# Kernel tuning notes

Measured on AMD Instinct MI355X. Metric: run time of the kernel, lower is better.

## Reference

```python
import jax, jax.numpy as jnp
import numpy as np

WS = 8          # window size
SS = 4          # shift size
NH = 4          # num heads
DIM = 128
RPE_HID = 512
MLP_HID = 512   # 4 * DIM
EPS = 1e-5


def _rel_coords_table(ws):
    h = np.arange(-(ws - 1), ws, dtype=np.float32)
    tbl = np.stack(np.meshgrid(h, h, indexing='ij'), axis=-1)  # [2ws-1, 2ws-1, 2]
    tbl = tbl / (ws - 1) * 8.0
    tbl = np.sign(tbl) * np.log2(np.abs(tbl) + 1.0) / np.log2(8.0)
    return jnp.asarray(tbl, dtype=jnp.float32)


def _rel_pos_index(ws):
    coords = np.stack(np.meshgrid(np.arange(ws), np.arange(ws), indexing='ij'))  # [2, ws, ws]
    cf = coords.reshape(2, -1)
    rel = (cf[:, :, None] - cf[:, None, :]).transpose(1, 2, 0).astype(np.int64)  # [N, N, 2]
    rel[..., 0] += ws - 1
    rel[..., 1] += ws - 1
    rel[..., 0] *= 2 * ws - 1
    return jnp.asarray(rel.sum(-1))  # [N, N]


def _attn_mask(H, W, ws, ss):
    img = np.zeros((H, W), np.float32)
    cnt = 0
    for hsl in (slice(0, -ws), slice(-ws, -ss), slice(-ss, None)):
        for wsl in (slice(0, -ws), slice(-ws, -ss), slice(-ss, None)):
            img[hsl, wsl] = cnt
            cnt += 1
    mw = img.reshape(H // ws, ws, W // ws, ws).transpose(0, 2, 1, 3).reshape(-1, ws * ws)
    diff = mw[:, None, :] - mw[:, :, None]
    return jnp.asarray(np.where(diff != 0, -100.0, 0.0).astype(np.float32))  # [nW, N, N]


def _layernorm(x, w, b):
    mu = x.mean(-1, keepdims=True)
    var = ((x - mu) ** 2).mean(-1, keepdims=True)
    return (x - mu) * jax.lax.rsqrt(var + EPS) * w + b


def setup_inputs() -> dict:
    key = jax.random.key(0)
    ks = jax.random.split(key, 16)
    s = 0.02
    return {
        'x': jax.random.normal(ks[0], (32, 4096, DIM), jnp.float32),
        'qkv_w': jax.random.normal(ks[1], (3 * DIM, DIM), jnp.float32) * s,
        'qkv_b': jnp.zeros((3 * DIM,), jnp.float32),
        'proj_w': jax.random.normal(ks[2], (DIM, DIM), jnp.float32) * s,
        'proj_b': jnp.zeros((DIM,), jnp.float32),
        'rpe_w1': jax.random.normal(ks[3], (RPE_HID, 2), jnp.float32) * s,
        'rpe_b1': jnp.zeros((RPE_HID,), jnp.float32),
        'rpe_w2': jax.random.normal(ks[4], (NH, RPE_HID), jnp.float32) * s,
        'norm1_w': jnp.ones((DIM,), jnp.float32),
        'norm1_b': jnp.zeros((DIM,), jnp.float32),
        'fc1_w': jax.random.normal(ks[5], (MLP_HID, DIM), jnp.float32) * s,
        'fc1_b': jnp.zeros((MLP_HID,), jnp.float32),
        'fc2_w': jax.random.normal(ks[6], (DIM, MLP_HID), jnp.float32) * s,
        'fc2_b': jnp.zeros((DIM,), jnp.float32),
        'norm2_w': jnp.ones((DIM,), jnp.float32),
        'norm2_b': jnp.zeros((DIM,), jnp.float32),
        'H': 64,
        'W': 64,
    }


def reference(x, qkv_w, qkv_b, proj_w, proj_b, rpe_w1, rpe_b1, rpe_w2,
              norm1_w, norm1_b, fc1_w, fc1_b, fc2_w, fc2_b, norm2_w, norm2_b, H, W):
    B, L, C = x.shape
    N = WS * WS
    hd = C // NH
    scale = hd ** -0.5
    nWh, nWw = H // WS, W // WS
    nW = nWh * nWw

    # ---- shifted window partition ----
    xs = x.reshape(B, H, W, C)
    xs = jnp.roll(xs, shift=(-SS, -SS), axis=(1, 2))
    xw = xs.reshape(B, nWh, WS, nWw, WS, C).transpose(0, 1, 3, 2, 4, 5).reshape(-1, N, C)

    # ---- window attention ----
    qkv = xw @ qkv_w.T + qkv_b                              # [B*nW, N, 3C]
    qkv = qkv.reshape(-1, N, 3, NH, hd).transpose(2, 0, 3, 1, 4)
    q, k, v = qkv[0], qkv[1], qkv[2]                        # [B*nW, NH, N, hd]
    attn = jnp.einsum('whnd,whmd->whnm', q * scale, k)      # [B*nW, NH, N, N]

    # continuous relative position bias via MLP on log-spaced coords
    tbl = _rel_coords_table(WS)                             # [2ws-1, 2ws-1, 2]
    t = jax.nn.relu(tbl @ rpe_w1.T + rpe_b1) @ rpe_w2.T     # [2ws-1, 2ws-1, NH]
    t = t.reshape(-1, NH)
    rel_idx = _rel_pos_index(WS)                            # [N, N]
    bias = t[rel_idx].transpose(2, 0, 1)                    # [NH, N, N]
    attn = attn + bias[None]

    # shift mask
    mask = _attn_mask(H, W, WS, SS)                         # [nW, N, N]
    attn = attn.reshape(B, nW, NH, N, N) + mask[None, :, None]
    attn = jax.nn.softmax(attn, axis=-1).reshape(-1, NH, N, N)

    out = jnp.einsum('whnm,whmd->whnd', attn, v)            # [B*nW, NH, N, hd]
    out = out.transpose(0, 2, 1, 3).reshape(-1, N, C)
    out = out @ proj_w.T + proj_b

    # ---- window reverse + unshift ----
    out = out.reshape(B, nWh, nWw, WS, WS, C).transpose(0, 1, 3, 2, 4, 5).reshape(B, H, W, C)
    out = jnp.roll(out, shift=(SS, SS), axis=(1, 2)).reshape(B, L, C)

    # ---- post-norm residual ----
    x = x + _layernorm(out, norm1_w, norm1_b)

    # ---- MLP (GELU exact) + post-norm residual ----
    h = jax.nn.gelu(x @ fc1_w.T + fc1_b, approximate=False)
    h = h @ fc2_w.T + fc2_b
    x = x + _layernorm(h, norm2_w, norm2_b)
    return x
```

## Files before the change

kernel.cpp:

```cpp
#include <hip/hip_runtime.h>
#include <hip/hip_bf16.h>

typedef __attribute__((ext_vector_type(8))) short short8_t;
typedef __attribute__((ext_vector_type(4))) float f32x4_t;
typedef __attribute__((ext_vector_type(2))) float f32x2_t;

#define NHEAD 4
#define SCALE 0.17677669529663687f

#define OFF_W    0L
#define OFF_TBL  393216L
#define OFF_QKV  458752L
#define OFF_X1   458752L
#define OFF_H    67567616L
#define OFF_ATTN 101122048L
#define OFF_PROJ 134676480L

__device__ __forceinline__ unsigned short f2bf(float f){
  unsigned int u = __float_as_uint(f);
  u += 0x7FFFu + ((u >> 16) & 1u);
  return (unsigned short)(u >> 16);
}
__device__ __forceinline__ float bf2f(unsigned short s){
  return __uint_as_float(((unsigned int)s) << 16);
}

__device__ __forceinline__ int win_row_to_orig(int r){
  int win = r >> 6, n = r & 63;
  int b = win >> 6, wh = (win >> 3) & 7, ww = win & 7;
  int hs = wh*8 + (n >> 3), wsv = ww*8 + (n & 7);
  return (b << 12) + (((hs + 4) & 63) << 6) + ((wsv + 4) & 63);
}

__global__ __launch_bounds__(256) void prep_kernel(
    const float* __restrict__ qkv_w, const float* __restrict__ proj_w,
    const float* __restrict__ fc1_w, const float* __restrict__ fc2_w,
    const float* __restrict__ rpe_w1, const float* __restrict__ rpe_b1,
    const float* __restrict__ rpe_w2,
    unsigned short* __restrict__ wbf, float* __restrict__ tbl)
{
  if (blockIdx.x == 0) {
    int t = threadIdx.x;
    if (t < 225) {
      int a = t / 15, b = t % 15;
      float v0 = (float)(a - 7) * (8.0f / 7.0f);
      float v1 = (float)(b - 7) * (8.0f / 7.0f);
      float c0 = (v0 > 0.f ? 1.f : (v0 < 0.f ? -1.f : 0.f)) * log2f(fabsf(v0) + 1.f) * (1.0f/3.0f);
      float c1 = (v1 > 0.f ? 1.f : (v1 < 0.f ? -1.f : 0.f)) * log2f(fabsf(v1) + 1.f) * (1.0f/3.0f);
      float a0 = 0.f, a1 = 0.f, a2 = 0.f, a3 = 0.f;
      for (int k = 0; k < 512; k++){
        float h = c0 * rpe_w1[2*k] + c1 * rpe_w1[2*k+1] + rpe_b1[k];
        h = fmaxf(h, 0.f);
        a0 += h * rpe_w2[k];
        a1 += h * rpe_w2[512 + k];
        a2 += h * rpe_w2[1024 + k];
        a3 += h * rpe_w2[1536 + k];
      }
      tbl[t] = a0; tbl[225 + t] = a1; tbl[450 + t] = a2; tbl[675 + t] = a3;
    }
  } else {
    int e = (blockIdx.x - 1) * 256 + threadIdx.x;
    float v;
    if (e < 49152)       v = qkv_w[e];
    else if (e < 65536)  v = proj_w[e - 49152];
    else if (e < 131072) v = fc1_w[e - 65536];
    else                 v = fc2_w[e - 131072];
    wbf[e] = f2bf(v);
  }
}

template<int N, int K, int AMODE, int EPI>
__global__ __launch_bounds__(256) void gemm_kernel(
    const void* __restrict__ Ap, const unsigned short* __restrict__ Bw,
    const float* __restrict__ bias, void* __restrict__ Out)
{
  constexpr int NT = N / 16;
  constexpr int KC = K / 32;
  __shared__ __align__(16) unsigned short bs[N * 40];
  int lane = threadIdx.x & 63;
  int wave = threadIdx.x >> 6;
  int m0 = blockIdx.x * 64 + wave * 16;
  int l15 = lane & 15;
  int kg  = lane >> 4;
  int arow = m0 + l15;
  int ag = (AMODE == 1) ? win_row_to_orig(arow) : arow;

  f32x4_t acc[NT];
#pragma unroll
  for (int t = 0; t < NT; t++) acc[t] = (f32x4_t){0.f, 0.f, 0.f, 0.f};

  for (int kc = 0; kc < KC; ++kc){
    if (kc) __syncthreads();
    for (int e = threadIdx.x; e < N * 4; e += 256){
      int n = e >> 2, k8 = e & 3;
      short8_t v = *(const short8_t*)(Bw + n * K + kc * 32 + k8 * 8);
      *(short8_t*)(&bs[n * 40 + k8 * 8]) = v;
    }
    __syncthreads();

    short8_t af;
    if (AMODE == 2) {
      af = *(const short8_t*)((const unsigned short*)Ap + (long)ag * K + kc * 32 + kg * 8);
    } else {
      const float* ap = (const float*)Ap + (long)ag * K + kc * 32 + kg * 8;
      f32x4_t a0 = *(const f32x4_t*)ap;
      f32x4_t a1 = *(const f32x4_t*)(ap + 4);
      union { short8_t v; unsigned short u[8]; } pk;
      pk.u[0] = f2bf(a0[0]); pk.u[1] = f2bf(a0[1]); pk.u[2] = f2bf(a0[2]); pk.u[3] = f2bf(a0[3]);
      pk.u[4] = f2bf(a1[0]); pk.u[5] = f2bf(a1[1]); pk.u[6] = f2bf(a1[2]); pk.u[7] = f2bf(a1[3]);
      af = pk.v;
    }
#pragma unroll
    for (int t = 0; t < NT; t++){
      short8_t bf = *(const short8_t*)(&bs[(t * 16 + l15) * 40 + kg * 8]);
      acc[t] = __builtin_amdgcn_mfma_f32_16x16x32_bf16(af, bf, acc[t], 0, 0, 0);
    }
  }

  int orow[4];
#pragma unroll
  for (int i = 0; i < 4; i++){
    int r = m0 + kg * 4 + i;
    orow[i] = (EPI == 1) ? win_row_to_orig(r) : r;
  }
#pragma unroll
  for (int t = 0; t < NT; t++){
    int col = t * 16 + l15;
    float bv = bias[col];
#pragma unroll
    for (int i = 0; i < 4; i++){
      float v = acc[t][i] + bv;
      if (EPI == 0) {
        ((unsigned short*)Out)[(long)orow[i] * N + col] = f2bf(v);
      } else if (EPI == 1) {
        ((float*)Out)[(long)orow[i] * N + col] = v;
      } else if (EPI == 2) {
        float g = 0.5f * v * (1.f + erff(v * 0.70710678118f));
        ((unsigned short*)Out)[(long)orow[i] * N + col] = f2bf(g);
      } else {
        ((float*)Out)[(long)orow[i] * N + col] = v;
      }
    }
  }
}

__global__ __launch_bounds__(256) void attn_kernel(
    const unsigned short* __restrict__ qkv, const float* __restrict__ tbl,
    unsigned short* __restrict__ outp)
{
  __shared__ __align__(16) unsigned short vt[NHEAD][32][72];
  __shared__ __align__(16) unsigned short pl[NHEAD][16][72];
  __shared__ float tl[900];
  int win  = blockIdx.x;
  int head = threadIdx.x >> 6;
  int lane = threadIdx.x & 63;
  int l15 = lane & 15, kg = lane >> 4;

  for (int e = threadIdx.x; e < 900; e += 256) tl[e] = tbl[e];

  const unsigned short* qbase = qkv + (long)win * 64 * 384;

  {
    const unsigned short* vp = qbase + lane * 384 + 256 + head * 32;
#pragma unroll
    for (int d0 = 0; d0 < 4; d0++){
      union { short8_t v; unsigned short u[8]; } pk;
      pk.v = *(const short8_t*)(vp + d0 * 8);
#pragma unroll
      for (int j = 0; j < 8; j++)
        vt[head][d0 * 8 + j][lane] = pk.u[j];
    }
  }

  short8_t kf[4];
#pragma unroll
  for (int nt = 0; nt < 4; nt++)
    kf[nt] = *(const short8_t*)(qbase + (nt * 16 + l15) * 384 + 128 + head * 32 + kg * 8);

  __syncthreads();

  short8_t bvf[2][2];
#pragma unroll
  for (int dt = 0; dt < 2; dt++)
#pragma unroll
    for (int ks = 0; ks < 2; ks++)
      bvf[dt][ks] = *(const short8_t*)(&vt[head][dt * 16 + l15][ks * 32 + kg * 8]);

  const float* tlh = tl + head * 225;
  bool wh7 = ((win >> 3) & 7) == 7;
  bool ww7 = (win & 7) == 7;
  bool crq_lt = (kg & 1) == 0;
  bool crm_lt = (l15 & 7) < 4;
  int  t3m_lo = l15 >> 3;
  int  dj0 = (kg & 1) * 4 - (l15 & 7) + 7;

#pragma unroll
  for (int mt = 0; mt < 4; mt++){
    short8_t qf = *(const short8_t*)(qbase + (mt * 16 + l15) * 384 + head * 32 + kg * 8);
    f32x4_t sacc[4];
#pragma unroll
    for (int nt = 0; nt < 4; nt++)
      sacc[nt] = __builtin_amdgcn_mfma_f32_16x16x32_bf16(qf, kf[nt], (f32x4_t){0.f,0.f,0.f,0.f}, 0, 0, 0);

    int t3q = mt * 2 + (kg >> 1);
    bool rrq_lt = t3q < 4;
    float p[4][4];
#pragma unroll
    for (int nt = 0; nt < 4; nt++){
      int t3m = nt * 2 + t3m_lo;
      const float* bp = tlh + (t3q - t3m + 7) * 15 + dj0;
      bool masked = (wh7 && (rrq_lt != (t3m < 4))) || (ww7 && (crq_lt != crm_lt));
      float mterm = masked ? -100.f : 0.f;
#pragma unroll
      for (int ii = 0; ii < 4; ii++){
        float s = sacc[nt][ii] * SCALE + bp[ii] + mterm;
        p[nt][ii] = __expf(s);
      }
    }
    float inv[4];
#pragma unroll
    for (int ii = 0; ii < 4; ii++){
      float sm = (p[0][ii] + p[1][ii]) + (p[2][ii] + p[3][ii]);
      sm += __shfl_xor(sm, 1); sm += __shfl_xor(sm, 2);
      sm += __shfl_xor(sm, 4); sm += __shfl_xor(sm, 8);
      inv[ii] = 1.f / sm;
    }
#pragma unroll
    for (int nt = 0; nt < 4; nt++)
#pragma unroll
      for (int ii = 0; ii < 4; ii++)
        pl[head][kg * 4 + ii][nt * 16 + l15] = f2bf(p[nt][ii]);

    asm volatile("s_waitcnt lgkmcnt(0)" ::: "memory");

    f32x4_t oacc[2] = {{0.f,0.f,0.f,0.f},{0.f,0.f,0.f,0.f}};
#pragma unroll
    for (int ks = 0; ks < 2; ks++){
      short8_t pa = *(const short8_t*)(&pl[head][l15][ks * 32 + kg * 8]);
#pragma unroll
      for (int dt = 0; dt < 2; dt++)
        oacc[dt] = __builtin_amdgcn_mfma_f32_16x16x32_bf16(pa, bvf[dt][ks], oacc[dt], 0, 0, 0);
    }

    unsigned short* op = outp + ((long)(win * 64 + mt * 16 + kg * 4)) * 128 + head * 32;
#pragma unroll
    for (int ii = 0; ii < 4; ii++)
#pragma unroll
      for (int dt = 0; dt < 2; dt++)
        op[ii * 128 + dt * 16 + l15] = f2bf(oacc[dt][ii] * inv[ii]);
  }
}

__global__ __launch_bounds__(256) void ln_residual_kernel(
    const float* in, const float* __restrict__ res,
    const float* __restrict__ w, const float* __restrict__ b, float* out)
{
  int row = blockIdx.x * 4 + (threadIdx.x >> 6);
  int lane = threadIdx.x & 63;
  long base = (long)row * 128 + lane * 2;
  f32x2_t v = *(const f32x2_t*)(in + base);
  float sm = v[0] + v[1];
#pragma unroll
  for (int off = 1; off < 64; off <<= 1) sm += __shfl_xor(sm, off);
  float mu = sm * 0.0078125f;
  float d0 = v[0] - mu, d1 = v[1] - mu;
  float qv = d0 * d0 + d1 * d1;
#pragma unroll
  for (int off = 1; off < 64; off <<= 1) qv += __shfl_xor(qv, off);
  float rs = rsqrtf(qv * 0.0078125f + 1e-5f);
  f32x2_t r = *(const f32x2_t*)(res + base);
  f32x2_t o;
  o[0] = r[0] + d0 * rs * w[lane*2]     + b[lane*2];
  o[1] = r[1] + d1 * rs * w[lane*2 + 1] + b[lane*2 + 1];
  *(f32x2_t*)(out + base) = o;
}

extern "C" void kernel_launch(void* const* d_in, const int* in_sizes, int n_in,
                              void* d_out, int out_size, void* d_ws, size_t ws_size,
                              hipStream_t stream)
{
  (void)in_sizes; (void)n_in; (void)out_size; (void)ws_size;
  const float* x      = (const float*)d_in[0];
  const float* qkv_w  = (const float*)d_in[1];
  const float* qkv_b  = (const float*)d_in[2];
  const float* proj_w = (const float*)d_in[3];
  const float* proj_b = (const float*)d_in[4];
  const float* rpe_w1 = (const float*)d_in[5];
  const float* rpe_b1 = (const float*)d_in[6];
  const float* rpe_w2 = (const float*)d_in[7];
  const float* n1w    = (const float*)d_in[8];
  const float* n1b    = (const float*)d_in[9];
  const float* fc1_w  = (const float*)d_in[10];
  const float* fc1_b  = (const float*)d_in[11];
  const float* fc2_w  = (const float*)d_in[12];
  const float* fc2_b  = (const float*)d_in[13];
  const float* n2w    = (const float*)d_in[14];
  const float* n2b    = (const float*)d_in[15];

  char* ws = (char*)d_ws;
  unsigned short* Wbf   = (unsigned short*)(ws + OFF_W);
  float*          tblp  = (float*)(ws + OFF_TBL);
  unsigned short* qkvp  = (unsigned short*)(ws + OFF_QKV);
  unsigned short* attnp = (unsigned short*)(ws + OFF_ATTN);
  float*          projp = (float*)(ws + OFF_PROJ);
  float*          x1p   = (float*)(ws + OFF_X1);
  unsigned short* hp    = (unsigned short*)(ws + OFF_H);
  float*          yp    = (float*)d_out;

  prep_kernel<<<769, 256, 0, stream>>>(qkv_w, proj_w, fc1_w, fc2_w, rpe_w1, rpe_b1, rpe_w2, Wbf, tblp);
  gemm_kernel<384, 128, 1, 0><<<2048, 256, 0, stream>>>(x, Wbf, qkv_b, qkvp);
  attn_kernel<<<2048, 256, 0, stream>>>(qkvp, tblp, attnp);
  gemm_kernel<128, 128, 2, 1><<<2048, 256, 0, stream>>>(attnp, Wbf + 49152, proj_b, projp);
  ln_residual_kernel<<<32768, 256, 0, stream>>>(projp, x, n1w, n1b, x1p);
  gemm_kernel<512, 128, 0, 2><<<2048, 256, 0, stream>>>(x1p, Wbf + 65536, fc1_b, hp);
  gemm_kernel<128, 512, 2, 3><<<2048, 256, 0, stream>>>(hp, Wbf + 131072, fc2_b, yp);
  ln_residual_kernel<<<32768, 256, 0, stream>>>(yp, x1p, n2w, n2b, (float*)d_out);
}
```

Measured before the change: 508.8 us.

## Fuse LayerNorm residual into GEMM epilogues and restructure GEMMs to register tiling

Replaces the shared-memory-staged GEMM with register-tiled kernels: one keeps a 64-row A tile in registers and streams B from global, the other computes full 128-column rows so bias, LayerNorm and residual add run in its epilogue. This removes both standalone LN kernels and the fp32 round-trips of the projection and fc2 outputs. The intermediate x1 is stored as bf16 and reused as both the fc1 input and the residual, which lowers precision of the residual path. Exact erf GELU is swapped for a polynomial approximation. LayerNorm variance now uses the single-pass E[x²]-mu² formula.

```diff
diff --git a/kernel.cpp b/kernel.cpp
--- a/kernel.cpp
+++ b/kernel.cpp
@@ -11,10 +11,9 @@
 #define OFF_W    0L
 #define OFF_TBL  393216L
 #define OFF_QKV  458752L
-#define OFF_X1   458752L
-#define OFF_H    67567616L
+#define OFF_H    458752L
 #define OFF_ATTN 101122048L
-#define OFF_PROJ 134676480L
+#define OFF_X1BF 134676480L
 
 __device__ __forceinline__ unsigned short f2bf(float f){
   unsigned int u = __float_as_uint(f);
@@ -30,6 +29,17 @@
   int b = win >> 6, wh = (win >> 3) & 7, ww = win & 7;
   int hs = wh*8 + (n >> 3), wsv = ww*8 + (n & 7);
   return (b << 12) + (((hs + 4) & 63) << 6) + ((wsv + 4) & 63);
+}
+
+__device__ __forceinline__ float gelu_exact(float x){
+  float z  = x * 0.70710678118654752f;
+  float az = fabsf(z);
+  float t  = __builtin_amdgcn_rcpf(1.0f + 0.3275911f * az);
+  float poly = t*(0.254829592f + t*(-0.284496736f + t*(1.421413741f +
+               t*(-1.453152027f + t*1.061405429f))));
+  float er = 1.0f - poly * __expf(-z*z);
+  er = (z < 0.f) ? -er : er;
+  return 0.5f * x * (1.0f + er);
 }
 
 __global__ __launch_bounds__(256) void prep_kernel(
@@ -69,79 +79,158 @@
   }
 }
 
-template<int N, int K, int AMODE, int EPI>
-__global__ __launch_bounds__(256) void gemm_kernel(
+template<int N, int AMODE, int EPI>
+__global__ __launch_bounds__(256) void gemm_a_kernel(
     const void* __restrict__ Ap, const unsigned short* __restrict__ Bw,
-    const float* __restrict__ bias, void* __restrict__ Out)
-{
-  constexpr int NT = N / 16;
-  constexpr int KC = K / 32;
-  __shared__ __align__(16) unsigned short bs[N * 40];
+    const float* __restrict__ bias, unsigned short* __restrict__ Out)
+{
+  constexpr int K  = 128;
+  constexpr int NC = N / 32;
   int lane = threadIdx.x & 63;
   int wave = threadIdx.x >> 6;
-  int m0 = blockIdx.x * 64 + wave * 16;
-  int l15 = lane & 15;
-  int kg  = lane >> 4;
-  int arow = m0 + l15;
-  int ag = (AMODE == 1) ? win_row_to_orig(arow) : arow;
-
-  f32x4_t acc[NT];
-#pragma unroll
-  for (int t = 0; t < NT; t++) acc[t] = (f32x4_t){0.f, 0.f, 0.f, 0.f};
-
-  for (int kc = 0; kc < KC; ++kc){
-    if (kc) __syncthreads();
-    for (int e = threadIdx.x; e < N * 4; e += 256){
-      int n = e >> 2, k8 = e & 3;
-      short8_t v = *(const short8_t*)(Bw + n * K + kc * 32 + k8 * 8);
-      *(short8_t*)(&bs[n * 40 + k8 * 8]) = v;
-    }
-    __syncthreads();
-
-    short8_t af;
-    if (AMODE == 2) {
-      af = *(const short8_t*)((const unsigned short*)Ap + (long)ag * K + kc * 32 + kg * 8);
+  int l15 = lane & 15, kg = lane >> 4;
+  int m0 = (blockIdx.x * 4 + wave) * 64;
+
+  short8_t a[4][4];
+#pragma unroll
+  for (int mr = 0; mr < 4; mr++){
+    int r = m0 + mr*16 + l15;
+    if (AMODE == 1) r = win_row_to_orig(r);
+    if (AMODE == 2){
+      const unsigned short* ap = (const unsigned short*)Ap + (long)r * K + kg * 8;
+#pragma unroll
+      for (int kc = 0; kc < 4; kc++)
+        a[mr][kc] = *(const short8_t*)(ap + kc * 32);
     } else {
-      const float* ap = (const float*)Ap + (long)ag * K + kc * 32 + kg * 8;
-      f32x4_t a0 = *(const f32x4_t*)ap;
-      f32x4_t a1 = *(const f32x4_t*)(ap + 4);
-      union { short8_t v; unsigned short u[8]; } pk;
-      pk.u[0] = f2bf(a0[0]); pk.u[1] = f2bf(a0[1]); pk.u[2] = f2bf(a0[2]); pk.u[3] = f2bf(a0[3]);
-      pk.u[4] = f2bf(a1[0]); pk.u[5] = f2bf(a1[1]); pk.u[6] = f2bf(a1[2]); pk.u[7] = f2bf(a1[3]);
-      af = pk.v;
-    }
-#pragma unroll
-    for (int t = 0; t < NT; t++){
-      short8_t bf = *(const short8_t*)(&bs[(t * 16 + l15) * 40 + kg * 8]);
-      acc[t] = __builtin_amdgcn_mfma_f32_16x16x32_bf16(af, bf, acc[t], 0, 0, 0);
-    }
-  }
-
-  int orow[4];
-#pragma unroll
-  for (int i = 0; i < 4; i++){
-    int r = m0 + kg * 4 + i;
-    orow[i] = (EPI == 1) ? win_row_to_orig(r) : r;
-  }
-#pragma unroll
-  for (int t = 0; t < NT; t++){
-    int col = t * 16 + l15;
-    float bv = bias[col];
+      const float* ap = (const float*)Ap + (long)r * K + kg * 8;
+#pragma unroll
+      for (int kc = 0; kc < 4; kc++){
+        f32x4_t a0 = *(const f32x4_t*)(ap + kc * 32);
+        f32x4_t a1 = *(const f32x4_t*)(ap + kc * 32 + 4);
+        union { short8_t v; unsigned short u[8]; } pk;
+        pk.u[0] = f2bf(a0[0]); pk.u[1] = f2bf(a0[1]); pk.u[2] = f2bf(a0[2]); pk.u[3] = f2bf(a0[3]);
+        pk.u[4] = f2bf(a1[0]); pk.u[5] = f2bf(a1[1]); pk.u[6] = f2bf(a1[2]); pk.u[7] = f2bf(a1[3]);
+        a[mr][kc] = pk.v;
+      }
+    }
+  }
+
+  const unsigned short* bp0 = Bw + (long)l15 * K + kg * 8;
+
+#pragma unroll 2
+  for (int nc = 0; nc < NC; nc++){
+    short8_t b[2][4];
+#pragma unroll
+    for (int nr = 0; nr < 2; nr++)
+#pragma unroll
+      for (int kc = 0; kc < 4; kc++)
+        b[nr][kc] = *(const short8_t*)(bp0 + (long)(nc*32 + nr*16) * K + kc * 32);
+
+    f32x4_t acc[4][2];
+#pragma unroll
+    for (int mr = 0; mr < 4; mr++)
+#pragma unroll
+      for (int nr = 0; nr < 2; nr++) acc[mr][nr] = (f32x4_t){0.f,0.f,0.f,0.f};
+#pragma unroll
+    for (int kc = 0; kc < 4; kc++)
+#pragma unroll
+      for (int mr = 0; mr < 4; mr++)
+#pragma unroll
+        for (int nr = 0; nr < 2; nr++)
+          acc[mr][nr] = __builtin_amdgcn_mfma_f32_16x16x32_bf16(a[mr][kc], b[nr][kc], acc[mr][nr], 0, 0, 0);
+
+#pragma unroll
+    for (int nr = 0; nr < 2; nr++){
+      int col = nc*32 + nr*16 + l15;
+      float bv = bias[col];
+#pragma unroll
+      for (int mr = 0; mr < 4; mr++)
+#pragma unroll
+        for (int i = 0; i < 4; i++){
+          float v = acc[mr][nr][i] + bv;
+          if (EPI == 2) v = gelu_exact(v);
+          Out[(long)(m0 + mr*16 + kg*4 + i) * N + col] = f2bf(v);
+        }
+    }
+  }
+}
+
+template<int K, int SCATTER, int RESBF, int OUTBF>
+__global__ __launch_bounds__(256) void gemm_b_ln_kernel(
+    const unsigned short* __restrict__ Ap, const unsigned short* __restrict__ Bw,
+    const float* __restrict__ bias,
+    const float* __restrict__ lnw, const float* __restrict__ lnb,
+    const void* __restrict__ Res, void* __restrict__ OutP)
+{
+  constexpr int KC = K / 32;
+  int lane = threadIdx.x & 63;
+  int wave = threadIdx.x >> 6;
+  int l15 = lane & 15, kg = lane >> 4;
+  int m0 = (blockIdx.x * 4 + wave) * 32;
+
+  f32x4_t acc[2][8];
+#pragma unroll
+  for (int mr = 0; mr < 2; mr++)
+#pragma unroll
+    for (int nt = 0; nt < 8; nt++) acc[mr][nt] = (f32x4_t){0.f,0.f,0.f,0.f};
+
+  const unsigned short* ap0 = Ap + (long)(m0 + l15) * K + kg * 8;
+  const unsigned short* bp0 = Bw + (long)l15 * K + kg * 8;
+
+#pragma unroll 2
+  for (int kc = 0; kc < KC; kc++){
+    short8_t a0 = *(const short8_t*)(ap0 + kc * 32);
+    short8_t a1 = *(const short8_t*)(ap0 + 16 * K + kc * 32);
+    short8_t b[8];
+#pragma unroll
+    for (int nt = 0; nt < 8; nt++)
+      b[nt] = *(const short8_t*)(bp0 + (long)nt * 16 * K + kc * 32);
+#pragma unroll
+    for (int nt = 0; nt < 8; nt++)
+      acc[0][nt] = __builtin_amdgcn_mfma_f32_16x16x32_bf16(a0, b[nt], acc[0][nt], 0, 0, 0);
+#pragma unroll
+    for (int nt = 0; nt < 8; nt++)
+      acc[1][nt] = __builtin_amdgcn_mfma_f32_16x16x32_bf16(a1, b[nt], acc[1][nt], 0, 0, 0);
+  }
+
+  float bv[8], wv[8], bb[8];
+#pragma unroll
+  for (int nt = 0; nt < 8; nt++){
+    int col = nt*16 + l15;
+    bv[nt] = bias[col]; wv[nt] = lnw[col]; bb[nt] = lnb[col];
+  }
+
+#pragma unroll
+  for (int mr = 0; mr < 2; mr++)
 #pragma unroll
     for (int i = 0; i < 4; i++){
-      float v = acc[t][i] + bv;
-      if (EPI == 0) {
-        ((unsigned short*)Out)[(long)orow[i] * N + col] = f2bf(v);
-      } else if (EPI == 1) {
-        ((float*)Out)[(long)orow[i] * N + col] = v;
-      } else if (EPI == 2) {
-        float g = 0.5f * v * (1.f + erff(v * 0.70710678118f));
-        ((unsigned short*)Out)[(long)orow[i] * N + col] = f2bf(g);
-      } else {
-        ((float*)Out)[(long)orow[i] * N + col] = v;
-      }
-    }
-  }
+      float v[8];
+      float s1 = 0.f, s2 = 0.f;
+#pragma unroll
+      for (int nt = 0; nt < 8; nt++){
+        v[nt] = acc[mr][nt][i] + bv[nt];
+        s1 += v[nt]; s2 += v[nt]*v[nt];
+      }
+      s1 += __shfl_xor(s1, 1); s2 += __shfl_xor(s2, 1);
+      s1 += __shfl_xor(s1, 2); s2 += __shfl_xor(s2, 2);
+      s1 += __shfl_xor(s1, 4); s2 += __shfl_xor(s2, 4);
+      s1 += __shfl_xor(s1, 8); s2 += __shfl_xor(s2, 8);
+      float mu = s1 * 0.0078125f;
+      float var = s2 * 0.0078125f - mu * mu;
+      float rs = rsqrtf(var + 1e-5f);
+      int row = m0 + mr*16 + kg*4 + i;
+      int orow = SCATTER ? win_row_to_orig(row) : row;
+      long rb = (long)orow * 128;
+#pragma unroll
+      for (int nt = 0; nt < 8; nt++){
+        int col = nt*16 + l15;
+        float r = RESBF ? bf2f(((const unsigned short*)Res)[rb + col])
+                        : ((const float*)Res)[rb + col];
+        float o = r + (v[nt] - mu) * rs * wv[nt] + bb[nt];
+        if (OUTBF) ((unsigned short*)OutP)[rb + col] = f2bf(o);
+        else       ((float*)OutP)[rb + col] = o;
+      }
+    }
 }
 
 __global__ __launch_bounds__(256) void attn_kernel(
@@ -249,30 +338,6 @@
       for (int dt = 0; dt < 2; dt++)
         op[ii * 128 + dt * 16 + l15] = f2bf(oacc[dt][ii] * inv[ii]);
   }
-}
-
-__global__ __launch_bounds__(256) void ln_residual_kernel(
-    const float* in, const float* __restrict__ res,
-    const float* __restrict__ w, const float* __restrict__ b, float* out)
-{
-  int row = blockIdx.x * 4 + (threadIdx.x >> 6);
-  int lane = threadIdx.x & 63;
-  long base = (long)row * 128 + lane * 2;
-  f32x2_t v = *(const f32x2_t*)(in + base);
-  float sm = v[0] + v[1];
-#pragma unroll
-  for (int off = 1; off < 64; off <<= 1) sm += __shfl_xor(sm, off);
-  float mu = sm * 0.0078125f;
-  float d0 = v[0] - mu, d1 = v[1] - mu;
-  float qv = d0 * d0 + d1 * d1;
-#pragma unroll
-  for (int off = 1; off < 64; off <<= 1) qv += __shfl_xor(qv, off);
-  float rs = rsqrtf(qv * 0.0078125f + 1e-5f);
-  f32x2_t r = *(const f32x2_t*)(res + base);
-  f32x2_t o;
-  o[0] = r[0] + d0 * rs * w[lane*2]     + b[lane*2];
-  o[1] = r[1] + d1 * rs * w[lane*2 + 1] + b[lane*2 + 1];
-  *(f32x2_t*)(out + base) = o;
 }
 
 extern "C" void kernel_launch(void* const* d_in, const int* in_sizes, int n_in,
@@ -302,17 +367,15 @@
   float*          tblp  = (float*)(ws + OFF_TBL);
   unsigned short* qkvp  = (unsigned short*)(ws + OFF_QKV);
   unsigned short* attnp = (unsigned short*)(ws + OFF_ATTN);
-  float*          projp = (float*)(ws + OFF_PROJ);
-  float*          x1p   = (float*)(ws + OFF_X1);
+  unsigned short* x1bf  = (unsigned short*)(ws + OFF_X1BF);
   unsigned short* hp    = (unsigned short*)(ws + OFF_H);
-  float*          yp    = (float*)d_out;
 
   prep_kernel<<<769, 256, 0, stream>>>(qkv_w, proj_w, fc1_w, fc2_w, rpe_w1, rpe_b1, rpe_w2, Wbf, tblp);
-  gemm_kernel<384, 128, 1, 0><<<2048, 256, 0, stream>>>(x, Wbf, qkv_b, qkvp);
+  gemm_a_kernel<384, 1, 0><<<512, 256, 0, stream>>>(x, Wbf, qkv_b, qkvp);
   attn_kernel<<<2048, 256, 0, stream>>>(qkvp, tblp, attnp);
-  gemm_kernel<128, 128, 2, 1><<<2048, 256, 0, stream>>>(attnp, Wbf + 49152, proj_b, projp);
-  ln_residual_kernel<<<32768, 256, 0, stream>>>(projp, x, n1w, n1b, x1p);
-  gemm_kernel<512, 128, 0, 2><<<2048, 256, 0, stream>>>(x1p, Wbf + 65536, fc1_b, hp);
-  gemm_kernel<128, 512, 2, 3><<<2048, 256, 0, stream>>>(hp, Wbf + 131072, fc2_b, yp);
-  ln_residual_kernel<<<32768, 256, 0, stream>>>(yp, x1p, n2w, n2b, (float*)d_out);
-}
+  gemm_b_ln_kernel<128, 1, 0, 1><<<1024, 256, 0, stream>>>(
+      attnp, Wbf + 49152, proj_b, n1w, n1b, x, x1bf);
+  gemm_a_kernel<512, 2, 2><<<512, 256, 0, stream>>>(x1bf, Wbf + 65536, fc1_b, hp);
+  gemm_b_ln_kernel<512, 0, 1, 0><<<1024, 256, 0, stream>>>(
+      hp, Wbf + 131072, fc2_b, n2w, n2b, x1bf, d_out);
+}
```

New measurement: 438.4 us. 13.8% less time.
